# Kernel tuning notes

Measured on AMD Instinct MI355X. Metric: run time of the kernel, lower is better.

Reference implementation:

```python
import jax, jax.numpy as jnp
from jax import lax
import numpy as np

R = 4            # search_range
B, H, W, C = 8, 192, 192, 64
CV = (2 * R + 1) ** 2          # 81 cost-volume channels
CIN0 = CV + 2 * C              # concat(cost, prv, nxt) channels = 209
FILTERS = (128, 64, 32, 16)
DN = ('NHWC', 'HWIO', 'NHWC')
EPS = 1e-3                     # Keras BatchNormalization default epsilon


def setup_inputs() -> dict:
    key = jax.random.key(0)
    ks = iter(jax.random.split(key, 32))
    inp = {}
    inp['prv'] = jax.random.normal(next(ks), (B, H, W, C), jnp.float32)
    inp['nxt'] = jax.random.normal(next(ks), (B, H, W, C), jnp.float32)
    cin = CIN0
    for i, f in enumerate(FILTERS):
        inp[f'dw{i}'] = jax.random.normal(next(ks), (3, 3, 1, cin), jnp.float32) / np.sqrt(9.0)
        inp[f'pw{i}'] = jax.random.normal(next(ks), (1, 1, cin, f), jnp.float32) / np.sqrt(cin)
        inp[f'b{i}'] = jnp.zeros((f,), jnp.float32)
        cin = f
    inp['bn_gamma'] = jnp.ones((cin,), jnp.float32)
    inp['bn_beta'] = jnp.zeros((cin,), jnp.float32)
    inp['bn_mean'] = jnp.zeros((cin,), jnp.float32)
    inp['bn_var'] = jnp.ones((cin,), jnp.float32)
    inp['flow_w'] = jax.random.normal(next(ks), (3, 3, cin, 2), jnp.float32) / np.sqrt(9.0 * cin)
    return inp


def mish(x):
    return x * jnp.tanh(jax.nn.softplus(x))


def cost_volume(prv, nxt):
    # pad nxt by R on spatial dims, correlate over (2R+1)^2 shifts
    pad = jnp.pad(nxt, ((0, 0), (R, R), (R, R), (0, 0)))
    vols = []
    for i in range(2 * R + 1):           # fixed 9x9 offset set (not a data dim)
        for j in range(2 * R + 1):
            roi = lax.slice(pad, (0, i, j, 0), (B, i + H, j + W, C))
            vols.append(jnp.mean(prv * roi, axis=-1))
    cv = jnp.stack(vols, axis=-1)        # [B,H,W,81]
    return jax.nn.leaky_relu(cv, 0.1)


def sep_conv(x, dw, pw, b):
    cin = x.shape[-1]
    y = lax.conv_general_dilated(x, dw, (1, 1), 'SAME',
                                 dimension_numbers=DN, feature_group_count=cin)
    y = lax.conv_general_dilated(y, pw, (1, 1), 'SAME', dimension_numbers=DN) + b
    return mish(y)


def reference(prv, nxt, dw0, pw0, b0, dw1, pw1, b1, dw2, pw2, b2, dw3, pw3, b3,
              bn_gamma, bn_beta, bn_mean, bn_var, flow_w):
    cost = cost_volume(prv, nxt)
    x = jnp.concatenate([cost, prv, nxt], axis=-1)   # [B,H,W,209]
    for dw, pw, b in ((dw0, pw0, b0), (dw1, pw1, b1), (dw2, pw2, b2), (dw3, pw3, b3)):
        x = sep_conv(x, dw, pw, b)
    # BatchNorm (inference: moving statistics)
    x = (x - bn_mean) * (bn_gamma / jnp.sqrt(bn_var + EPS)) + bn_beta
    flow = lax.conv_general_dilated(x, flow_w, (1, 1), 'SAME', dimension_numbers=DN)
    scale = (float(H) ** 2 + float(W) ** 2) ** 0.5
    return scale * flow
```

## Files before the change

kernel.cpp:

```cpp
#include <hip/hip_runtime.h>
#include <hip/hip_bf16.h>

#define BB 8
#define HH 192
#define WW 192
#define CC0 64
#define NPIX (BB*HH*WW)
#define NCV 81
#define CVP 96

typedef __attribute__((ext_vector_type(8))) short short8;
typedef __attribute__((ext_vector_type(4))) short short4v;
typedef __attribute__((ext_vector_type(4))) float f32x4;

__device__ __forceinline__ float bf2f(short s) {
    union { unsigned u; float f; } x; x.u = ((unsigned)(unsigned short)s) << 16; return x.f;
}
__device__ __forceinline__ short f2bf(float f) {
    __hip_bfloat16 h = __float2bfloat16(f);
    return *reinterpret_cast<short*>(&h);
}
__device__ __forceinline__ void cvt8(const short8 iv, float* fv) {
    const int* ip = (const int*)&iv;
#pragma unroll
    for (int e = 0; e < 4; ++e) {
        union { unsigned u; float f; } lo, hi;
        lo.u = ((unsigned)ip[e]) << 16;
        hi.u = ((unsigned)ip[e]) & 0xffff0000u;
        fv[2 * e] = lo.f; fv[2 * e + 1] = hi.f;
    }
}

__device__ __forceinline__ float mish_f(float v) {
    if (v > 20.0f) return v;
    const float u = __expf(v);
    const float n = u * (u + 2.0f);
    return v * n / (n + 2.0f);
}

__global__ __launch_bounds__(256) void prep_kernel(
    const float* __restrict__ dw0, const float* __restrict__ pw0,
    const float* __restrict__ dw1, const float* __restrict__ pw1,
    const float* __restrict__ dw2, const float* __restrict__ pw2,
    const float* __restrict__ dw3, const float* __restrict__ pw3,
    __hip_bfloat16* __restrict__ wout)
{
    const int u = blockIdx.x * 256 + threadIdx.x;
    if (u >= 43456) return;
    float v = 0.f;
    if (u < 2016) {
        const int t = u / 224, c = u % 224;
        if (c < 64)       v = dw0[t*209 + 81  + c];
        else if (c < 128) v = dw0[t*209 + 145 + (c-64)];
        else if (c < 209) v = dw0[t*209 + (c-128)];
    } else if (u < 3168) {
        const int r = u-2016, t = r/128, c = r%128; v = dw1[t*128+c];
    } else if (u < 3744) {
        const int r = u-3168, t = r/64, c = r%64; v = dw2[t*64+c];
    } else if (u < 4032) {
        const int r = u-3744, t = r/32, c = r%32; v = dw3[t*32+c];
    } else if (u < 32704) {
        const int r = u-4032, n = r/224, c = r%224;
        if (c < 64)       v = pw0[(81+c)*128 + n];
        else if (c < 128) v = pw0[(145+(c-64))*128 + n];
        else if (c < 209) v = pw0[(c-128)*128 + n];
    } else if (u < 40896) {
        const int r = u-32704, n = r/128, c = r%128; v = pw1[c*64 + n];
    } else if (u < 42944) {
        const int r = u-40896, n = r/64, c = r%64; v = pw2[c*32 + n];
    } else {
        const int r = u-42944, n = r/32, c = r%32; v = pw3[c*16 + n];
    }
    wout[u] = __float2bfloat16(v);
}

__global__ __launch_bounds__(256) void prep2_kernel(
    const float* __restrict__ dw0, const float* __restrict__ dw1,
    const float* __restrict__ dw2, const float* __restrict__ dw3,
    const float* __restrict__ bn_g, const float* __restrict__ bn_b,
    const float* __restrict__ bn_m, const float* __restrict__ bn_v,
    const float* __restrict__ fw, float* __restrict__ fout)
{
    const int u = blockIdx.x * 256 + threadIdx.x;
    if (u >= 4338) return;
    float v = 0.f;
    if (u < 2016) {
        const int t = u / 224, c = u % 224;
        if (c < 64)       v = dw0[t*209 + 81  + c];
        else if (c < 128) v = dw0[t*209 + 145 + (c-64)];
        else if (c < 209) v = dw0[t*209 + (c-128)];
    } else if (u < 3168) {
        const int r = u-2016, t = r/128, c = r%128; v = dw1[t*128+c];
    } else if (u < 3744) {
        const int r = u-3168, t = r/64, c = r%64; v = dw2[t*64+c];
    } else if (u < 4032) {
        const int r = u-3744, t = r/32, c = r%32; v = dw3[t*32+c];
    } else if (u < 4320) {
        const int r = u-4032, t = r/32, rem = r%32, c = rem >> 1, s = rem & 1;
        const float sc = bn_g[c] * rsqrtf(bn_v[c] + 1e-3f);
        v = sc * fw[t*32 + c*2 + s];
    } else {
        const int r = u-4320, t = r/2, s = r%2;
        float a = 0.f;
        for (int c = 0; c < 16; ++c) {
            const float sc = bn_g[c] * rsqrtf(bn_v[c] + 1e-3f);
            const float sh = bn_b[c] - bn_m[c] * sc;
            a += sh * fw[t*32 + c*2 + s];
        }
        v = a;
    }
    fout[u] = v;
}

template<int UNIFIED>
__global__ __launch_bounds__(256) void cost_mfma_kernel(
    const float* __restrict__ prv, const float* __restrict__ nxt,
    __hip_bfloat16* __restrict__ xout)
{
    constexpr int OST   = UNIFIED ? 224 : CVP;
    constexpr int CVOFF = UNIFIED ? 128 : 0;

    __shared__ __align__(16) short sNxt[80][70];
    __shared__ __align__(16) short sCv[64][96];

    const int tid  = threadIdx.x;
    const int lane = tid & 63;
    const int wv   = tid >> 6;
    const int ln15 = lane & 15;
    const int kq   = lane >> 4;

    const int bx = blockIdx.x;
    const int tw = bx % 3;
    const int h  = (bx / 3) % HH;
    const int b  = bx / (3 * HH);
    const int w0 = tw * 64;

    {
        const short8 z = {0,0,0,0,0,0,0,0};
        for (int t = 0; t < 3; ++t) {
            const int idx = tid + t * 256;
            const int px = idx / 12, c8 = idx % 12;
            *(short8*)&sCv[px][c8 * 8] = z;
        }
    }

    short8 af0, af1;
    {
        const int apx = w0 + wv * 16 + ln15;
        const float* ap = prv + (((size_t)b * HH + h) * WW + apx) * CC0 + kq * 8;
        const float4 x0 = *(const float4*)(ap);
        const float4 x1 = *(const float4*)(ap + 4);
        const float4 x2 = *(const float4*)(ap + 32);
        const float4 x3 = *(const float4*)(ap + 36);
        af0[0]=f2bf(x0.x); af0[1]=f2bf(x0.y); af0[2]=f2bf(x0.z); af0[3]=f2bf(x0.w);
        af0[4]=f2bf(x1.x); af0[5]=f2bf(x1.y); af0[6]=f2bf(x1.z); af0[7]=f2bf(x1.w);
        af1[0]=f2bf(x2.x); af1[1]=f2bf(x2.y); af1[2]=f2bf(x2.z); af1[3]=f2bf(x2.w);
        af1[4]=f2bf(x3.x); af1[5]=f2bf(x3.y); af1[6]=f2bf(x3.z); af1[7]=f2bf(x3.w);
    }

    const int m0 = wv * 16;
    short* outp = (short*)xout + (((size_t)b * HH + h) * WW + w0) * OST;

    for (int r = 0; r < 9; ++r) {
        const int y = h - 4 + r;
        const bool yok = ((unsigned)y < (unsigned)HH);
        __syncthreads();
        if (yok) {
            const float* rowp = nxt + (((size_t)b * HH + y) * WW) * CC0;
#pragma unroll
            for (int t = 0; t < 5; ++t) {
                const int idx = tid + t * 256;
                const int px  = idx >> 4;
                const int c4  = idx & 15;
                const int gw  = w0 - 4 + px;
                float4 v = make_float4(0.f, 0.f, 0.f, 0.f);
                if ((unsigned)gw < (unsigned)WW)
                    v = *(const float4*)(rowp + (size_t)gw * CC0 + c4 * 4);
                short4v sv;
                sv[0]=f2bf(v.x); sv[1]=f2bf(v.y); sv[2]=f2bf(v.z); sv[3]=f2bf(v.w);
                *(short4v*)&sNxt[px][c4 * 4] = sv;
            }
        }
        __syncthreads();
        if (!yok) continue;

#pragma unroll
        for (int j = 0; j < 2; ++j) {
            const short* bp = &sNxt[m0 + j * 16 + ln15][kq * 8];
            const short8 b0 = *(const short8*)bp;
            const short8 b1 = *(const short8*)(bp + 32);
            f32x4 acc = {0.f, 0.f, 0.f, 0.f};
            acc = __builtin_amdgcn_mfma_f32_16x16x32_bf16(af0, b0, acc, 0, 0, 0);
            acc = __builtin_amdgcn_mfma_f32_16x16x32_bf16(af1, b1, acc, 0, 0, 0);
#pragma unroll
            for (int rr = 0; rr < 4; ++rr) {
                const int m  = kq * 4 + rr;
                const int dj = j * 16 + ln15 - m;
                if ((unsigned)dj < 9u) {
                    float mv = acc[rr] * (1.0f / 64.0f);
                    mv = (mv > 0.f) ? mv : 0.1f * mv;
                    sCv[m0 + m][r * 9 + dj] = f2bf(mv);
                }
            }
        }
        if (UNIFIED && r == 4) {
#pragma unroll
            for (int t = 0; t < 2; ++t) {
                const int u = tid + t * 256;
                const int px = u >> 3, cg = u & 7;
                *(short8*)(outp + (size_t)px * OST + 64 + cg * 8) =
                    *(const short8*)&sNxt[4 + px][cg * 8];
            }
        }
    }

    __syncthreads();
#pragma unroll
    for (int t = 0; t < 3; ++t) {
        const int idx = tid + t * 256;
        const int px = idx / 12, c8 = idx % 12;
        *(short8*)(outp + (size_t)px * OST + CVOFF + c8 * 8) = *(const short8*)&sCv[px][c8 * 8];
    }
    if (UNIFIED) {
        short* sf = &sNxt[0][0];
        {
            const int px = wv * 16 + ln15;
            *(short8*)&sf[px * 64 + kq * 8] = af0;
            *(short8*)&sf[px * 64 + kq * 8 + 32] = af1;
        }
        __syncthreads();
#pragma unroll
        for (int t = 0; t < 2; ++t) {
            const int u = tid + t * 256;
            const int px = u >> 3, cg = u & 7;
            *(short8*)(outp + (size_t)px * OST + cg * 8) = *(const short8*)&sf[px * 64 + cg * 8];
        }
    }
}

template<int KP, int COUT, int MODE>
__global__ __launch_bounds__(256) void sepconv_mfma(
    const __hip_bfloat16* __restrict__ in,
    const float* __restrict__ prv, const float* __restrict__ nxt,
    const float* __restrict__ dwf,
    const __hip_bfloat16* __restrict__ Bt,
    const float* __restrict__ bias,
    __hip_bfloat16* __restrict__ out)
{
    constexpr int NT  = COUT / 16;
    constexpr int WGN = (NT >= 2) ? 2 : 1;
    constexpr int WGM = 4 / WGN;
    constexpr int TM  = 8 / WGM;
    constexpr int TN  = NT / WGN;

    __shared__ __align__(16) short sIn[6][34][32];
    __shared__ __align__(16) short sA[4][128][8];
    __shared__ __align__(16) short sB[4][COUT][8];

    const int tid  = threadIdx.x;
    const int lane = tid & 63;
    const int wv   = tid >> 6;
    const int ln15 = lane & 15;
    const int kq   = lane >> 4;
    const int wm   = wv % WGM;
    const int wn   = wv / WGM;

    const int bx = blockIdx.x;
    const int tw = bx % 6;
    const int th = (bx / 6) % 48;
    const int bb = bx / 288;
    const int w0 = tw * 32, h0 = th * 4;

    const int dkbu = __builtin_amdgcn_readfirstlane(wv);
    const int dww  = lane & 31;
    const int dhh  = (lane >> 5) * 2;

    f32x4 acc[TM][TN] = {};

    for (int k0 = 0; k0 < KP; k0 += 32) {
        for (int u = tid; u < 816; u += 256) {
            const int kb = u & 3;
            const int p  = u >> 2;
            const int iw = p % 34, ih = p / 34;
            const int gw = w0 - 1 + iw, gh = h0 - 1 + ih;
            short8 v = {0,0,0,0,0,0,0,0};
            if ((unsigned)gw < (unsigned)WW && (unsigned)gh < (unsigned)HH) {
                const size_t pix = ((size_t)bb * HH + gh) * WW + gw;
                const int c0 = k0 + kb * 8;
                if (MODE == 0) {
                    v = *(const short8*)((const short*)in + pix * KP + c0);
                } else {
                    if (c0 < 64) {
                        const float4* s = (const float4*)(prv + pix * 64 + c0);
                        const float4 a = s[0], bq = s[1];
                        v[0]=f2bf(a.x);  v[1]=f2bf(a.y);  v[2]=f2bf(a.z);  v[3]=f2bf(a.w);
                        v[4]=f2bf(bq.x); v[5]=f2bf(bq.y); v[6]=f2bf(bq.z); v[7]=f2bf(bq.w);
                    } else if (c0 < 128) {
                        const float4* s = (const float4*)(nxt + pix * 64 + (c0 - 64));
                        const float4 a = s[0], bq = s[1];
                        v[0]=f2bf(a.x);  v[1]=f2bf(a.y);  v[2]=f2bf(a.z);  v[3]=f2bf(a.w);
                        v[4]=f2bf(bq.x); v[5]=f2bf(bq.y); v[6]=f2bf(bq.z); v[7]=f2bf(bq.w);
                    } else {
                        v = *(const short8*)((const short*)in + pix * CVP + (c0 - 128));
                    }
                }
            }
            *(short8*)&sIn[ih][iw][kb * 8] = v;
        }
        for (int u = tid; u < COUT * 4; u += 256) {
            const int n = u >> 2, kb = u & 3;
            short8 v = *(const short8*)((const short*)Bt + (size_t)n * KP + k0 + kb * 8);
            *(short8*)&sB[kb][n ^ (kb << 2)][0] = v;
        }
        __syncthreads();

        {
            const float* wrow = dwf + k0 + dkbu * 8;
            float r0[8] = {0,0,0,0,0,0,0,0};
            float r1[8] = {0,0,0,0,0,0,0,0};
#pragma unroll
            for (int dy = 0; dy < 4; ++dy) {
#pragma unroll
                for (int dx = 0; dx < 3; ++dx) {
                    const short8 iv = *(const short8*)&sIn[dhh + dy][dww + dx][dkbu * 8];
                    float fv[8];
                    cvt8(iv, fv);
                    if (dy < 3) {
#pragma unroll
                        for (int j = 0; j < 8; ++j)
                            r0[j] += fv[j] * wrow[(dy * 3 + dx) * KP + j];
                    }
                    if (dy >= 1) {
#pragma unroll
                        for (int j = 0; j < 8; ++j)
                            r1[j] += fv[j] * wrow[((dy - 1) * 3 + dx) * KP + j];
                    }
                }
            }
            const int px0 = dhh * 32 + dww;
            short8 o0, o1;
#pragma unroll
            for (int j = 0; j < 8; ++j) { o0[j] = f2bf(r0[j]); o1[j] = f2bf(r1[j]); }
            *(short8*)&sA[dkbu][px0 ^ (dkbu << 2)][0] = o0;
            *(short8*)&sA[dkbu][(px0 + 32) ^ (dkbu << 2)][0] = o1;
        }
        __syncthreads();

        short8 af[TM], bf8[TN];
#pragma unroll
        for (int i = 0; i < TM; ++i) {
            const int m = (wm * TM + i) * 16 + ln15;
            af[i] = *(const short8*)&sA[kq][m ^ (kq << 2)][0];
        }
#pragma unroll
        for (int j = 0; j < TN; ++j) {
            const int n = (wn * TN + j) * 16 + ln15;
            bf8[j] = *(const short8*)&sB[kq][n ^ (kq << 2)][0];
        }
#pragma unroll
        for (int i = 0; i < TM; ++i)
#pragma unroll
            for (int j = 0; j < TN; ++j)
                acc[i][j] = __builtin_amdgcn_mfma_f32_16x16x32_bf16(
                    af[i], bf8[j], acc[i][j], 0, 0, 0);
        __syncthreads();
    }

#pragma unroll
    for (int j = 0; j < TN; ++j) {
        const int n = (wn * TN + j) * 16 + ln15;
        const float bj = bias[n];
#pragma unroll
        for (int i = 0; i < TM; ++i) {
#pragma unroll
            for (int r = 0; r < 4; ++r) {
                const int m  = (wm * TM + i) * 16 + kq * 4 + r;
                const int gh = h0 + (m >> 5), gw = w0 + (m & 31);
                const size_t gp = ((size_t)bb * HH + gh) * WW + gw;
                out[gp * COUT + n] = __float2bfloat16(mish_f(acc[i][j][r] + bj));
            }
        }
    }
}

__global__ __launch_bounds__(256) void bn_flow_kernel(
    const __hip_bfloat16* __restrict__ xin,
    const float* __restrict__ fwp, const float* __restrict__ tbv,
    float* __restrict__ out)
{
    const int pix = blockIdx.x * 256 + threadIdx.x;
    const int wq  = pix % WW;
    const int hq  = (pix / WW) % HH;
    const int bq  = pix / (WW * HH);
    float a0 = 0.f, a1 = 0.f;
#pragma unroll
    for (int dy = -1; dy <= 1; ++dy) {
        const int yy = hq + dy;
        if ((unsigned)yy >= HH) continue;
#pragma unroll
        for (int dx = -1; dx <= 1; ++dx) {
            const int xx = wq + dx;
            if ((unsigned)xx >= WW) continue;
            const int t = (dy + 1) * 3 + (dx + 1);
            a0 += tbv[t * 2 + 0];
            a1 += tbv[t * 2 + 1];
            const short* xp = (const short*)xin + (((size_t)bq * HH + yy) * WW + xx) * 16;
            const short8 v0 = *(const short8*)xp;
            const short8 v1 = *(const short8*)(xp + 8);
            float x[16];
            cvt8(v0, x); cvt8(v1, x + 8);
            const float* wp = fwp + t * 32;
#pragma unroll
            for (int c = 0; c < 16; ++c) {
                a0 += x[c] * wp[c * 2 + 0];
                a1 += x[c] * wp[c * 2 + 1];
            }
        }
    }
    const float SC = sqrtf((float)(HH * HH + WW * WW));
    out[(size_t)pix * 2 + 0] = SC * a0;
    out[(size_t)pix * 2 + 1] = SC * a1;
}

extern "C" void kernel_launch(void* const* d_in, const int* in_sizes, int n_in,
                              void* d_out, int out_size, void* d_ws, size_t ws_size,
                              hipStream_t stream)
{
    const float* prv   = (const float*)d_in[0];
    const float* nxt   = (const float*)d_in[1];
    const float* dw0   = (const float*)d_in[2];
    const float* pw0   = (const float*)d_in[3];
    const float* b0    = (const float*)d_in[4];
    const float* dw1   = (const float*)d_in[5];
    const float* pw1   = (const float*)d_in[6];
    const float* b1    = (const float*)d_in[7];
    const float* dw2   = (const float*)d_in[8];
    const float* pw2   = (const float*)d_in[9];
    const float* b2    = (const float*)d_in[10];
    const float* dw3   = (const float*)d_in[11];
    const float* pw3   = (const float*)d_in[12];
    const float* b3    = (const float*)d_in[13];
    const float* bn_g  = (const float*)d_in[14];
    const float* bn_b  = (const float*)d_in[15];
    const float* bn_m  = (const float*)d_in[16];
    const float* bn_v  = (const float*)d_in[17];
    const float* fw    = (const float*)d_in[18];
    float* outp = (float*)d_out;

    const size_t N = (size_t)NPIX;
    __hip_bfloat16* ws = (__hip_bfloat16*)d_ws;

    const size_t need_uni = (N * 352 + 43456) * 2 + 4338 * 4;
    const bool uni = (ws_size >= need_uni);

    __hip_bfloat16* t1  = uni ? (ws + N * 224) : (ws + N * 96);
    __hip_bfloat16* wts = uni ? (ws + N * 352) : (ws + N * 224);
    __hip_bfloat16* t2  = ws;
    __hip_bfloat16* t3  = t1;
    __hip_bfloat16* t4  = ws + N * 64;
    __hip_bfloat16* Bt0 = wts + 4032;
    __hip_bfloat16* Bt1 = wts + 32704;
    __hip_bfloat16* Bt2 = wts + 40896;
    __hip_bfloat16* Bt3 = wts + 42944;
    float* fwt = (float*)(wts + 43456);

    prep_kernel<<<170, 256, 0, stream>>>(dw0, pw0, dw1, pw1, dw2, pw2, dw3, pw3, wts);
    prep2_kernel<<<17, 256, 0, stream>>>(dw0, dw1, dw2, dw3,
                                         bn_g, bn_b, bn_m, bn_v, fw, fwt);
    if (uni) {
        cost_mfma_kernel<1><<<3 * HH * BB, 256, 0, stream>>>(prv, nxt, ws);
        sepconv_mfma<224, 128, 0><<<2304, 256, 0, stream>>>(ws, nullptr, nullptr,
                                                            fwt, Bt0, b0, t1);
    } else {
        cost_mfma_kernel<0><<<3 * HH * BB, 256, 0, stream>>>(prv, nxt, ws);
        sepconv_mfma<224, 128, 1><<<2304, 256, 0, stream>>>(ws, prv, nxt,
                                                            fwt, Bt0, b0, t1);
    }
    sepconv_mfma<128, 64, 0><<<2304, 256, 0, stream>>>(t1, nullptr, nullptr,
                                                       fwt + 2016, Bt1, b1, t2);
    sepconv_mfma<64, 32, 0><<<2304, 256, 0, stream>>>(t2, nullptr, nullptr,
                                                      fwt + 3168, Bt2, b2, t3);
    sepconv_mfma<32, 16, 0><<<2304, 256, 0, stream>>>(t3, nullptr, nullptr,
                                                      fwt + 3744, Bt3, b3, t4);
    bn_flow_kernel<<<NPIX / 256, 256, 0, stream>>>(t4, fwt + 4032, fwt + 4320, outp);
}
```

Before: 549.6 us.

## Tile cost volume over 4 output rows with double-buffered nxt row loads

```diff
diff --git a/kernel.cpp b/kernel.cpp
--- a/kernel.cpp
+++ b/kernel.cpp
@@ -120,120 +120,171 @@
     constexpr int OST   = UNIFIED ? 224 : CVP;
     constexpr int CVOFF = UNIFIED ? 128 : 0;
 
-    __shared__ __align__(16) short sNxt[80][70];
-    __shared__ __align__(16) short sCv[64][96];
+    __shared__ __align__(16) short sNxt[2][48][70];
+    __shared__ __align__(16) short sCv[4][32][96];
 
     const int tid  = threadIdx.x;
     const int lane = tid & 63;
     const int wv   = tid >> 6;
     const int ln15 = lane & 15;
     const int kq   = lane >> 4;
+    const int mt   = wv & 1;
+    const int jt   = wv >> 1;
 
     const int bx = blockIdx.x;
-    const int tw = bx % 3;
-    const int h  = (bx / 3) % HH;
-    const int b  = bx / (3 * HH);
-    const int w0 = tw * 64;
+    const int tw = bx % 6;
+    const int th = (bx / 6) % 48;
+    const int b  = bx / 288;
+    const int w0 = tw * 32, h0 = th * 4;
 
     {
         const short8 z = {0,0,0,0,0,0,0,0};
-        for (int t = 0; t < 3; ++t) {
+#pragma unroll
+        for (int t = 0; t < 6; ++t) {
             const int idx = tid + t * 256;
-            const int px = idx / 12, c8 = idx % 12;
-            *(short8*)&sCv[px][c8 * 8] = z;
-        }
-    }
-
-    short8 af0, af1;
+            const int row = idx / 384, rem = idx % 384;
+            const int px = rem / 12, c8 = rem % 12;
+            *(short8*)&sCv[row][px][c8 * 8] = z;
+        }
+    }
+
+    short8 af0[4], af1[4];
     {
-        const int apx = w0 + wv * 16 + ln15;
-        const float* ap = prv + (((size_t)b * HH + h) * WW + apx) * CC0 + kq * 8;
-        const float4 x0 = *(const float4*)(ap);
-        const float4 x1 = *(const float4*)(ap + 4);
-        const float4 x2 = *(const float4*)(ap + 32);
-        const float4 x3 = *(const float4*)(ap + 36);
-        af0[0]=f2bf(x0.x); af0[1]=f2bf(x0.y); af0[2]=f2bf(x0.z); af0[3]=f2bf(x0.w);
-        af0[4]=f2bf(x1.x); af0[5]=f2bf(x1.y); af0[6]=f2bf(x1.z); af0[7]=f2bf(x1.w);
-        af1[0]=f2bf(x2.x); af1[1]=f2bf(x2.y); af1[2]=f2bf(x2.z); af1[3]=f2bf(x2.w);
-        af1[4]=f2bf(x3.x); af1[5]=f2bf(x3.y); af1[6]=f2bf(x3.z); af1[7]=f2bf(x3.w);
-    }
-
-    const int m0 = wv * 16;
-    short* outp = (short*)xout + (((size_t)b * HH + h) * WW + w0) * OST;
-
-    for (int r = 0; r < 9; ++r) {
-        const int y = h - 4 + r;
+        const int apx = w0 + mt * 16 + ln15;
+#pragma unroll
+        for (int r4 = 0; r4 < 4; ++r4) {
+            const float* ap = prv + (((size_t)b * HH + h0 + r4) * WW + apx) * CC0 + kq * 8;
+            const float4 x0 = *(const float4*)(ap);
+            const float4 x1 = *(const float4*)(ap + 4);
+            const float4 x2 = *(const float4*)(ap + 32);
+            const float4 x3 = *(const float4*)(ap + 36);
+            af0[r4][0]=f2bf(x0.x); af0[r4][1]=f2bf(x0.y); af0[r4][2]=f2bf(x0.z); af0[r4][3]=f2bf(x0.w);
+            af0[r4][4]=f2bf(x1.x); af0[r4][5]=f2bf(x1.y); af0[r4][6]=f2bf(x1.z); af0[r4][7]=f2bf(x1.w);
+            af1[r4][0]=f2bf(x2.x); af1[r4][1]=f2bf(x2.y); af1[r4][2]=f2bf(x2.z); af1[r4][3]=f2bf(x2.w);
+            af1[r4][4]=f2bf(x3.x); af1[r4][5]=f2bf(x3.y); af1[r4][6]=f2bf(x3.z); af1[r4][7]=f2bf(x3.w);
+        }
+    }
+
+    const int s_px = (tid & 0xFF) >> 4;
+
+    int cur = 0;
+    {
+        const int y0 = h0 - 4;
+        if ((unsigned)y0 < (unsigned)HH) {
+            const float* rowp = nxt + (((size_t)b * HH + y0) * WW) * CC0;
+#pragma unroll
+            for (int t = 0; t < 3; ++t) {
+                const int u = tid + t * 256;
+                if (u < 640) {
+                    const int px = u >> 4, c4 = u & 15;
+                    const int gw = w0 - 4 + px;
+                    float4 v = make_float4(0.f, 0.f, 0.f, 0.f);
+                    if ((unsigned)gw < (unsigned)WW)
+                        v = *(const float4*)(rowp + (size_t)gw * CC0 + c4 * 4);
+                    short4v sv;
+                    sv[0]=f2bf(v.x); sv[1]=f2bf(v.y); sv[2]=f2bf(v.z); sv[3]=f2bf(v.w);
+                    *(short4v*)&sNxt[0][px][c4 * 4] = sv;
+                }
+            }
+        }
+    }
+
+    const size_t obase_blk = (((size_t)b * HH + h0) * WW + w0);
+
+    for (int i = 0; i < 12; ++i) {
+        const int y = h0 - 4 + i;
         const bool yok = ((unsigned)y < (unsigned)HH);
         __syncthreads();
+
+        const int yn = y + 1;
+        const bool nok = (i < 11) && ((unsigned)yn < (unsigned)HH);
+        float4 sreg[3];
+        if (nok) {
+            const float* rowp = nxt + (((size_t)b * HH + yn) * WW) * CC0;
+#pragma unroll
+            for (int t = 0; t < 3; ++t) {
+                const int u = tid + t * 256;
+                sreg[t] = make_float4(0.f, 0.f, 0.f, 0.f);
+                if (u < 640) {
+                    const int px = u >> 4, c4 = u & 15;
+                    const int gw = w0 - 4 + px;
+                    if ((unsigned)gw < (unsigned)WW)
+                        sreg[t] = *(const float4*)(rowp + (size_t)gw * CC0 + c4 * 4);
+                }
+            }
+        }
+
         if (yok) {
-            const float* rowp = nxt + (((size_t)b * HH + y) * WW) * CC0;
-#pragma unroll
-            for (int t = 0; t < 5; ++t) {
-                const int idx = tid + t * 256;
-                const int px  = idx >> 4;
-                const int c4  = idx & 15;
-                const int gw  = w0 - 4 + px;
-                float4 v = make_float4(0.f, 0.f, 0.f, 0.f);
-                if ((unsigned)gw < (unsigned)WW)
-                    v = *(const float4*)(rowp + (size_t)gw * CC0 + c4 * 4);
-                short4v sv;
-                sv[0]=f2bf(v.x); sv[1]=f2bf(v.y); sv[2]=f2bf(v.z); sv[3]=f2bf(v.w);
-                *(short4v*)&sNxt[px][c4 * 4] = sv;
-            }
-        }
-        __syncthreads();
-        if (!yok) continue;
-
-#pragma unroll
-        for (int j = 0; j < 2; ++j) {
-            const short* bp = &sNxt[m0 + j * 16 + ln15][kq * 8];
+            const int nb = mt * 16 + jt * 16 + ln15;
+            const short* bp = &sNxt[cur][nb][kq * 8];
             const short8 b0 = *(const short8*)bp;
             const short8 b1 = *(const short8*)(bp + 32);
-            f32x4 acc = {0.f, 0.f, 0.f, 0.f};
-            acc = __builtin_amdgcn_mfma_f32_16x16x32_bf16(af0, b0, acc, 0, 0, 0);
-            acc = __builtin_amdgcn_mfma_f32_16x16x32_bf16(af1, b1, acc, 0, 0, 0);
-#pragma unroll
-            for (int rr = 0; rr < 4; ++rr) {
-                const int m  = kq * 4 + rr;
-                const int dj = j * 16 + ln15 - m;
-                if ((unsigned)dj < 9u) {
-                    float mv = acc[rr] * (1.0f / 64.0f);
-                    mv = (mv > 0.f) ? mv : 0.1f * mv;
-                    sCv[m0 + m][r * 9 + dj] = f2bf(mv);
+#pragma unroll
+            for (int r4 = 0; r4 < 4; ++r4) {
+                const int h = h0 + r4;
+                const int rband = y - h + 4;
+                if ((unsigned)rband <= 8u) {
+                    f32x4 acc = {0.f, 0.f, 0.f, 0.f};
+                    acc = __builtin_amdgcn_mfma_f32_16x16x32_bf16(af0[r4], b0, acc, 0, 0, 0);
+                    acc = __builtin_amdgcn_mfma_f32_16x16x32_bf16(af1[r4], b1, acc, 0, 0, 0);
+#pragma unroll
+                    for (int rr = 0; rr < 4; ++rr) {
+                        const int m_local = kq * 4 + rr;
+                        const int dj = jt * 16 + ln15 - m_local;
+                        if ((unsigned)dj < 9u) {
+                            float mv = acc[rr] * (1.0f / 64.0f);
+                            mv = (mv > 0.f) ? mv : 0.1f * mv;
+                            sCv[r4][mt * 16 + m_local][rband * 9 + dj] = f2bf(mv);
+                        }
+                    }
                 }
             }
-        }
-        if (UNIFIED && r == 4) {
-#pragma unroll
-            for (int t = 0; t < 2; ++t) {
+            if (UNIFIED && y >= h0 && y < h0 + 4) {
+                const int px_o = tid >> 3, cg = tid & 7;
+                short* op = (short*)xout + (((size_t)b * HH + y) * WW + w0 + px_o) * OST
+                            + 64 + cg * 8;
+                *(short8*)op = *(const short8*)&sNxt[cur][4 + px_o][cg * 8];
+            }
+        }
+
+        if (nok) {
+#pragma unroll
+            for (int t = 0; t < 3; ++t) {
                 const int u = tid + t * 256;
-                const int px = u >> 3, cg = u & 7;
-                *(short8*)(outp + (size_t)px * OST + 64 + cg * 8) =
-                    *(const short8*)&sNxt[4 + px][cg * 8];
-            }
-        }
+                if (u < 640) {
+                    const int px = u >> 4, c4 = u & 15;
+                    short4v sv;
+                    sv[0]=f2bf(sreg[t].x); sv[1]=f2bf(sreg[t].y);
+                    sv[2]=f2bf(sreg[t].z); sv[3]=f2bf(sreg[t].w);
+                    *(short4v*)&sNxt[cur ^ 1][px][c4 * 4] = sv;
+                }
+            }
+        }
+        cur ^= 1;
     }
 
     __syncthreads();
 #pragma unroll
-    for (int t = 0; t < 3; ++t) {
+    for (int t = 0; t < 6; ++t) {
         const int idx = tid + t * 256;
-        const int px = idx / 12, c8 = idx % 12;
-        *(short8*)(outp + (size_t)px * OST + CVOFF + c8 * 8) = *(const short8*)&sCv[px][c8 * 8];
+        const int row = idx / 384, rem = idx % 384;
+        const int px = rem / 12, c8 = rem % 12;
+        short* op = (short*)xout + (obase_blk + (size_t)row * WW + px) * OST + CVOFF + c8 * 8;
+        *(short8*)op = *(const short8*)&sCv[row][px][c8 * 8];
     }
     if (UNIFIED) {
-        short* sf = &sNxt[0][0];
-        {
-            const int px = wv * 16 + ln15;
-            *(short8*)&sf[px * 64 + kq * 8] = af0;
-            *(short8*)&sf[px * 64 + kq * 8 + 32] = af1;
-        }
-        __syncthreads();
-#pragma unroll
-        for (int t = 0; t < 2; ++t) {
+#pragma unroll
+        for (int t = 0; t < 4; ++t) {
             const int u = tid + t * 256;
-            const int px = u >> 3, cg = u & 7;
-            *(short8*)(outp + (size_t)px * OST + cg * 8) = *(const short8*)&sf[px * 64 + cg * 8];
+            const int row = u >> 8, px = (u >> 3) & 31, cg = u & 7;
+            const float* ap = prv + (obase_blk + (size_t)row * WW + px) * CC0 + cg * 8;
+            const float4 x0 = *(const float4*)(ap);
+            const float4 x1 = *(const float4*)(ap + 4);
+            short8 v;
+            v[0]=f2bf(x0.x); v[1]=f2bf(x0.y); v[2]=f2bf(x0.z); v[3]=f2bf(x0.w);
+            v[4]=f2bf(x1.x); v[5]=f2bf(x1.y); v[6]=f2bf(x1.z); v[7]=f2bf(x1.w);
+            short* op = (short*)xout + (obase_blk + (size_t)row * WW + px) * OST + cg * 8;
+            *(short8*)op = v;
         }
     }
 }
@@ -468,11 +519,11 @@
     prep2_kernel<<<17, 256, 0, stream>>>(dw0, dw1, dw2, dw3,
                                          bn_g, bn_b, bn_m, bn_v, fw, fwt);
     if (uni) {
-        cost_mfma_kernel<1><<<3 * HH * BB, 256, 0, stream>>>(prv, nxt, ws);
+        cost_mfma_kernel<1><<<2304, 256, 0, stream>>>(prv, nxt, ws);
         sepconv_mfma<224, 128, 0><<<2304, 256, 0, stream>>>(ws, nullptr, nullptr,
                                                             fwt, Bt0, b0, t1);
     } else {
-        cost_mfma_kernel<0><<<3 * HH * BB, 256, 0, stream>>>(prv, nxt, ws);
+        cost_mfma_kernel<0><<<2304, 256, 0, stream>>>(prv, nxt, ws);
         sepconv_mfma<224, 128, 1><<<2304, 256, 0, stream>>>(ws, prv, nxt,
                                                             fwt, Bt0, b0, t1);
     }
```

Measured after the change: 537.5 us. 2.2% less time.
